# Optimization experiments

Measured on AMD Instinct MI355X. Metric: run time of the kernel, lower is better.

Reference implementation:

```python
import jax, jax.numpy as jnp
from jax import lax
import numpy as np

B, D, P = 4096, 256, 512  # batch, encoded_space_dim (=d_prototypes), n_prototypes
BN_EPS = 1e-5  # torch BatchNorm eval with running_mean=0, running_var=1


def _conv(x, w, stride, pad):
    # x: NCHW, w: OIHW
    return lax.conv_general_dilated(x, w, (stride, stride), [(pad, pad), (pad, pad)],
                                    dimension_numbers=('NCHW', 'OIHW', 'NCHW'))


def _conv_t(x, w, stride, pad, out_pad):
    # torch ConvTranspose2d; w in torch layout [Cin, Cout, kh, kw]
    k = w.shape[2]
    wf = jnp.flip(w, (2, 3)).transpose(1, 0, 2, 3)  # -> OIHW, flipped
    lo = k - 1 - pad
    hi = k - 1 - pad + out_pad
    return lax.conv_general_dilated(x, wf, (1, 1), [(lo, hi), (lo, hi)],
                                    lhs_dilation=(stride, stride),
                                    dimension_numbers=('NCHW', 'OIHW', 'NCHW'))


def _bn(x, g, b):
    # eval-mode BatchNorm2d with running_mean=0, running_var=1
    s = g / jnp.sqrt(1.0 + BN_EPS)
    return x * s[None, :, None, None] + b[None, :, None, None]


def _bias(x, b):
    return x + b[None, :, None, None]


def setup_inputs() -> dict:
    key = jax.random.key(0)
    ks = jax.random.split(key, 32)
    n = jax.random.normal
    inp = {
        'x': jax.random.uniform(ks[0], (B, 1, 28, 28), jnp.float32),
        # encoder
        'w1': n(ks[1], (8, 1, 3, 3), jnp.float32) * 0.1, 'b1': jnp.zeros((8,), jnp.float32),
        'w2': n(ks[2], (16, 8, 3, 3), jnp.float32) * 0.1, 'b2': jnp.zeros((16,), jnp.float32),
        'g2': jnp.ones((16,), jnp.float32), 'bt2': jnp.zeros((16,), jnp.float32),
        'w3': n(ks[3], (D, 16, 3, 3), jnp.float32) * 0.1, 'b3': jnp.zeros((D,), jnp.float32),
        # prototypes (torch.rand init)
        'protolayer': jax.random.uniform(ks[4], (P, D, 1, 1), jnp.float32),
        # up layer (ConvTranspose2d(D, D, 5), torch layout [Cin,Cout,kh,kw])
        'wup': n(ks[5], (D, D, 5, 5), jnp.float32) * 0.02, 'bup': jnp.zeros((D,), jnp.float32),
        'gup': jnp.ones((D,), jnp.float32), 'btup': jnp.zeros((D,), jnp.float32),
        # decoder
        'wd1': n(ks[6], (D, 16, 3, 3), jnp.float32) * 0.05, 'bd1': jnp.zeros((16,), jnp.float32),
        'gd1': jnp.ones((16,), jnp.float32), 'btd1': jnp.zeros((16,), jnp.float32),
        'wd2': n(ks[7], (16, 8, 3, 3), jnp.float32) * 0.1, 'bd2': jnp.zeros((8,), jnp.float32),
        'gd2': jnp.ones((8,), jnp.float32), 'btd2': jnp.zeros((8,), jnp.float32),
        'wd3': n(ks[8], (8, 1, 3, 3), jnp.float32) * 0.1, 'bd3': jnp.zeros((1,), jnp.float32),
    }
    return inp


def reference(x, w1, b1, w2, b2, g2, bt2, w3, b3, protolayer,
              wup, bup, gup, btup,
              wd1, bd1, gd1, btd1, wd2, bd2, gd2, btd2, wd3, bd3):
    # ---- encoder: 28 -> 14 -> 7 -> 5 ----
    h = jax.nn.relu(_bias(_conv(x, w1, 2, 1), b1))
    h = jax.nn.relu(_bn(_bias(_conv(h, w2, 2, 1), b2), g2, bt2))
    h = jax.nn.relu(_bias(_conv(h, w3, 1, 0), b3))  # [B, D, 5, 5]

    # ---- l2 'convolution' with 1x1 prototypes ----
    p = protolayer[:, :, 0, 0]                                  # [P, D]
    x2_patch_sum = jnp.sum(h * h, axis=1)                       # ones-conv, 1x1 kernel -> channel sum [B,5,5]
    xp = jnp.einsum('bdhw,pd->bphw', h, p)                      # [B, P, 5, 5]
    p2 = jnp.sum(p * p, axis=1)                                 # [P]
    distances = jax.nn.relu(x2_patch_sum[:, None] - 2.0 * xp + p2[None, :, None, None])

    # min-pool over full spatial extent
    min_distances = jnp.min(distances, axis=(2, 3))             # [B, P]
    prototype_activations = -min_distances                      # 'linear' distance_2_similarity
    w = jax.nn.softmax(prototype_activations, axis=1)
    z = jnp.einsum('bp,pdkl->bdkl', w, protolayer)              # [B, D, 1, 1]

    # ---- up layer: 1 -> 5 ----
    z = jax.nn.relu(_bn(_bias(_conv_t(z, wup, 1, 0, 0), bup), gup, btup))

    # ---- decoder: 5 -> 7 -> 14 -> 28 ----
    h = jax.nn.relu(_bn(_bias(_conv_t(z, wd1, 1, 0, 0), bd1), gd1, btd1))
    h = jax.nn.relu(_bn(_bias(_conv_t(h, wd2, 2, 1, 1), bd2), gd2, btd2))
    out = jax.nn.sigmoid(_bias(_conv_t(h, wd3, 2, 1, 1), bd3))  # [B, 1, 28, 28]
    return out, min_distances
```

## Files before the change

kernel.cpp:

```cpp
#include <hip/hip_runtime.h>
#include <hip/hip_bf16.h>
#include <math.h>

#define NB 4096
#define DC 256
#define PC 512

typedef unsigned short ushort_t;
typedef __attribute__((ext_vector_type(4))) unsigned short us4;
typedef __attribute__((ext_vector_type(8))) unsigned short us8;
typedef __attribute__((ext_vector_type(8))) short s8v;
typedef __attribute__((ext_vector_type(4))) float f32x4;

__device__ __forceinline__ float bf16_to_f(ushort_t u) {
    union { unsigned int i; float f; } c;
    c.i = ((unsigned int)u) << 16;
    return c.f;
}
__device__ __forceinline__ ushort_t f2bf(float f) {
    union { float f; unsigned int u; } c; c.f = f;
    unsigned int r = c.u + 0x7fffu + ((c.u >> 16) & 1u);
    return (ushort_t)(r >> 16);
}

__global__ __launch_bounds__(256) void k_pre(
    const float* __restrict__ proto, float* __restrict__ p2,
    ushort_t* __restrict__ pfragHi, ushort_t* __restrict__ pfragLo,
    const float* __restrict__ w3, ushort_t* __restrict__ w3fH, ushort_t* __restrict__ w3fL,
    const float* __restrict__ w2, ushort_t* __restrict__ w2fH, ushort_t* __restrict__ w2fL,
    const float* __restrict__ wd1, ushort_t* __restrict__ wd1frag,
    const float* __restrict__ wup, ushort_t* __restrict__ wupfH, ushort_t* __restrict__ wupfL)
{
    int b = blockIdx.x, tid = threadIdx.x;
    __shared__ float red[256];
    if (b < 512) {
        int p = b, d = tid;
        float v = proto[p * DC + d];
        red[d] = v * v;
        __syncthreads();
        for (int s = 128; s > 0; s >>= 1) {
            if (d < s) red[d] += red[d + s];
            __syncthreads();
        }
        if (d == 0) p2[p] = red[0];
    } else if (b < 1024) {
        int idx = (b - 512) * 256 + tid;
        int j = idx & 7, l = (idx >> 3) & 63;
        int k0 = (idx >> 9) & 7, nt = idx >> 12;
        int n = nt * 16 + (l & 15);
        int k = k0 * 32 + (l >> 4) * 8 + j;
        float v = proto[n * DC + k];
        ushort_t hi = f2bf(v);
        pfragHi[idx] = hi;
        pfragLo[idx] = f2bf(v - bf16_to_f(hi));
    } else if (b < 1184) {
        int idx = (b - 1024) * 256 + tid;
        int j = idx & 7, l = (idx >> 3) & 63;
        int q = idx >> 9;
        int k0 = q % 5, nt = q / 5;
        int d = nt * 16 + (l & 15);
        int k = k0 * 32 + (l >> 4) * 8 + j;
        float v = (k < 144) ? w3[d * 144 + k] : 0.f;
        ushort_t hi = f2bf(v);
        w3fH[idx] = hi;
        w3fL[idx] = f2bf(v - bf16_to_f(hi));
    } else if (b < 1190) {
        int idx = (b - 1184) * 256 + tid;
        int j = idx & 7, l = (idx >> 3) & 63;
        int k0 = idx >> 9;
        int ch = l & 15;
        int k = k0 * 32 + (l >> 4) * 8 + j;
        float v = (k < 72) ? w2[ch * 72 + k] : 0.f;
        ushort_t hi = f2bf(v);
        w2fH[idx] = hi;
        w2fL[idx] = f2bf(v - bf16_to_f(hi));
    } else if (b < 1334) {
        int idx = (b - 1190) * 256 + tid;
        int j = idx & 7, l = (idx >> 3) & 63;
        int k0 = (idx >> 9) & 7, nt = idx >> 12;
        int n = nt * 16 + (l & 15);
        int k = k0 * 32 + (l >> 4) * 8 + j;
        wd1frag[idx] = f2bf(wd1[k * 144 + n]);
    } else {
        int idx = (b - 1334) * 256 + tid;
        int j = idx & 7, l = (idx >> 3) & 63;
        int k0 = (idx >> 9) & 7, nt = idx >> 12;
        int np = nt * 16 + (l & 15);
        int d = k0 * 32 + (l >> 4) * 8 + j;
        int pos = np >> 8, ch = np & 255;
        float v = wup[d * 6400 + ch * 25 + pos];
        ushort_t hi = f2bf(v);
        wupfH[idx] = hi;
        wupfL[idx] = f2bf(v - bf16_to_f(hi));
    }
}

__global__ __launch_bounds__(256) void k_pw2(
    const ushort_t* __restrict__ pfragHi, const ushort_t* __restrict__ pfragLo,
    const ushort_t* __restrict__ wupfH, const ushort_t* __restrict__ wupfL,
    ushort_t* __restrict__ PWfrag)
{
    int t = threadIdx.x;
    int w = t >> 6, l = t & 63, lr = l & 15, lg = l >> 4;
    int my = blockIdx.y;
    int ntb = blockIdx.x * 16 + w * 4;
    const s8v* AH = (const s8v*)pfragHi;
    const s8v* AL = (const s8v*)pfragLo;
    const s8v* BH = (const s8v*)wupfH;
    const s8v* BL = (const s8v*)wupfL;
    f32x4 acc[4];
#pragma unroll
    for (int q = 0; q < 4; q++) acc[q] = (f32x4){0.f, 0.f, 0.f, 0.f};
#pragma unroll
    for (int k0 = 0; k0 < 8; k0++) {
        s8v ah = AH[(my * 8 + k0) * 64 + l];
        s8v al = AL[(my * 8 + k0) * 64 + l];
#pragma unroll
        for (int q = 0; q < 4; q++) {
            s8v bh = BH[(size_t)((ntb + q) * 8 + k0) * 64 + l];
            s8v bl = BL[(size_t)((ntb + q) * 8 + k0) * 64 + l];
            acc[q] = __builtin_amdgcn_mfma_f32_16x16x32_bf16(ah, bh, acc[q], 0, 0, 0);
            acc[q] = __builtin_amdgcn_mfma_f32_16x16x32_bf16(al, bh, acc[q], 0, 0, 0);
            acc[q] = __builtin_amdgcn_mfma_f32_16x16x32_bf16(ah, bl, acc[q], 0, 0, 0);
        }
    }
#pragma unroll
    for (int q = 0; q < 4; q++) {
        int nt = ntb + q;
#pragma unroll
        for (int r = 0; r < 4; r++) {
            int p = my * 16 + lg * 4 + r;
            int k0p = p >> 5;
            int ll = ((p >> 3) & 3) * 16 + lr;
            int jj = p & 7;
            PWfrag[(((size_t)(nt * 16 + k0p) * 64) + ll) * 8 + jj] = f2bf(acc[q][r]);
        }
    }
}

__global__ __launch_bounds__(512) void k_enc1(
    const float* __restrict__ x,
    const float* __restrict__ w1, const float* __restrict__ b1,
    const ushort_t* __restrict__ w2fH, const ushort_t* __restrict__ w2fL,
    const float* __restrict__ b2,
    const float* __restrict__ g2, const float* __restrict__ bt2,
    const ushort_t* __restrict__ w3fH, const ushort_t* __restrict__ w3fL,
    const float* __restrict__ b3,
    ushort_t* __restrict__ h3g,
    float* __restrict__ x2g)
{
    int b = blockIdx.x;
    int t = threadIdx.x;
    int w = t >> 6, l = t & 63, lr = l & 15, lg = l >> 4;

    __shared__ __align__(16) unsigned char buf[25856];
    __shared__ float x2s[32];
    float* xb = (float*)buf;
    float* h1 = (float*)(buf + 3136);
    ushort_t* im2Hi = (ushort_t*)(buf + 9408);
    float* h2 = (float*)(buf + 22720);
    ushort_t* imHi = (ushort_t*)buf;

    const float bnr = rsqrtf(1.0f + 1e-5f);

    const float* xg = x + (size_t)b * 784;
    for (int i = t; i < 784; i += 512) xb[i] = xg[i];
    for (int i = t; i < 832; i += 512)
        ((float4*)(buf + 9408))[i] = (float4){0.f, 0.f, 0.f, 0.f};
    if (t < 32) x2s[t] = (t < 25) ? 0.f : 1e30f;
    __syncthreads();

    for (int o = t; o < 1568; o += 512) {
        int c = o / 196, r = o % 196, y = r / 14, xc = r % 14;
        float acc = b1[c];
        for (int sy = 0; sy < 3; sy++) {
            int iy = 2 * y - 1 + sy;
            if ((unsigned)iy >= 28u) continue;
            for (int sx = 0; sx < 3; sx++) {
                int ix = 2 * xc - 1 + sx;
                if ((unsigned)ix >= 28u) continue;
                acc += w1[c * 9 + sy * 3 + sx] * xb[iy * 28 + ix];
            }
        }
        float v = fmaxf(acc, 0.f);
        ushort_t hi = f2bf(v);
        int kb = c * 9;
        int yA, syA, xA, sxA, yB = 0, xB = 0;
        bool hasYB, hasXB;
        if (y & 1) { yA = y >> 1; syA = 2; yB = yA + 1; hasYB = (yB < 7); }
        else       { yA = y >> 1; syA = 1; hasYB = false; }
        if (xc & 1) { xA = xc >> 1; sxA = 2; xB = xA + 1; hasXB = (xB < 7); }
        else        { xA = xc >> 1; sxA = 1; hasXB = false; }
        im2Hi[(yA * 7 + xA) * 104 + kb + syA * 3 + sxA] = hi;
        if (hasXB) im2Hi[(yA * 7 + xB) * 104 + kb + syA * 3] = hi;
        if (hasYB) {
            im2Hi[(yB * 7 + xA) * 104 + kb + sxA] = hi;
            if (hasXB) im2Hi[(yB * 7 + xB) * 104 + kb] = hi;
        }
    }
    __syncthreads();

    if (w < 4) {
        f32x4 cc = {0, 0, 0, 0};
        const s8v* WH = (const s8v*)w2fH;
        const s8v* WL = (const s8v*)w2fL;
#pragma unroll
        for (int k0 = 0; k0 < 3; k0++) {
            s8v a0 = *(const s8v*)&im2Hi[(w * 16 + lr) * 104 + k0 * 32 + lg * 8];
            s8v bh = WH[k0 * 64 + l];
            s8v bl = WL[k0 * 64 + l];
            cc = __builtin_amdgcn_mfma_f32_16x16x32_bf16(a0, bh, cc, 0, 0, 0);
            cc = __builtin_amdgcn_mfma_f32_16x16x32_bf16(a0, bl, cc, 0, 0, 0);
        }
        int ch = lr;
        float s = g2[ch] * bnr, bb = b2[ch], bt = bt2[ch];
#pragma unroll
        for (int r = 0; r < 4; r++) {
            int pos = w * 16 + lg * 4 + r;
            if (pos < 49)
                h2[ch * 49 + pos] = fmaxf((cc[r] + bb) * s + bt, 0.f);
        }
    }
    __syncthreads();

    if (t < 16) imHi[3600 + t] = 0;
    for (int o = t; o < 784; o += 512) {
        float v = h2[o];
        int ci = o / 49, rr = o % 49, iy = rr / 7, ixp = rr % 7;
        ushort_t hi = f2bf(v);
        int kb = ci * 9;
#pragma unroll
        for (int sy = 0; sy < 3; sy++) {
            int py = iy - sy;
            if ((unsigned)py < 5u) {
#pragma unroll
                for (int sx = 0; sx < 3; sx++) {
                    int px = ixp - sx;
                    if ((unsigned)px < 5u)
                        imHi[(py * 5 + px) * 144 + kb + sy * 3 + sx] = hi;
                }
            }
        }
    }
    __syncthreads();

    {
        int nt0 = 2 * w;
        f32x4 c00 = {0,0,0,0}, c01 = {0,0,0,0}, c10 = {0,0,0,0}, c11 = {0,0,0,0};
        const s8v* WH = (const s8v*)w3fH;
        const s8v* WL = (const s8v*)w3fL;
#pragma unroll
        for (int k0 = 0; k0 < 5; k0++) {
            s8v ah0 = *(const s8v*)&imHi[lr * 144 + k0 * 32 + lg * 8];
            s8v ah1 = *(const s8v*)&imHi[(16 + lr) * 144 + k0 * 32 + lg * 8];
            s8v bh0 = WH[(nt0 * 5 + k0) * 64 + l];
            s8v bl0 = WL[(nt0 * 5 + k0) * 64 + l];
            s8v bh1 = WH[((nt0 + 1) * 5 + k0) * 64 + l];
            s8v bl1 = WL[((nt0 + 1) * 5 + k0) * 64 + l];
            c00 = __builtin_amdgcn_mfma_f32_16x16x32_bf16(ah0, bh0, c00, 0, 0, 0);
            c10 = __builtin_amdgcn_mfma_f32_16x16x32_bf16(ah1, bh0, c10, 0, 0, 0);
            c00 = __builtin_amdgcn_mfma_f32_16x16x32_bf16(ah0, bl0, c00, 0, 0, 0);
            c10 = __builtin_amdgcn_mfma_f32_16x16x32_bf16(ah1, bl0, c10, 0, 0, 0);
            c01 = __builtin_amdgcn_mfma_f32_16x16x32_bf16(ah0, bh1, c01, 0, 0, 0);
            c11 = __builtin_amdgcn_mfma_f32_16x16x32_bf16(ah1, bh1, c11, 0, 0, 0);
            c01 = __builtin_amdgcn_mfma_f32_16x16x32_bf16(ah0, bl1, c01, 0, 0, 0);
            c11 = __builtin_amdgcn_mfma_f32_16x16x32_bf16(ah1, bl1, c11, 0, 0, 0);
        }
        ushort_t* hg = h3g + (size_t)b * 6400;
#pragma unroll
        for (int q = 0; q < 2; q++) {
            int d = (nt0 + q) * 16 + lr;
            float bb = b3[d];
            f32x4 cm0 = q ? c01 : c00;
            f32x4 cm1 = q ? c11 : c10;
#pragma unroll
            for (int mt = 0; mt < 2; mt++) {
                f32x4 cv = mt ? cm1 : cm0;
#pragma unroll
                for (int r = 0; r < 4; r++) {
                    int pos = mt * 16 + lg * 4 + r;
                    if (pos < 25) {
                        float h = fmaxf(cv[r] + bb, 0.f);
                        ushort_t hi = f2bf(h);
                        float hh = bf16_to_f(hi);
                        hg[pos * 256 + d] = hi;
                        float sq = hh * hh;
                        sq += __shfl_xor(sq, 1);
                        sq += __shfl_xor(sq, 2);
                        sq += __shfl_xor(sq, 4);
                        sq += __shfl_xor(sq, 8);
                        if (lr == 0) atomicAdd(&x2s[pos], sq);
                    }
                }
            }
        }
    }
    __syncthreads();
    if (t < 32) x2g[(size_t)b * 32 + t] = x2s[t];
}

__global__ __launch_bounds__(1024) void k_enc2(
    const ushort_t* __restrict__ h3g,
    const float* __restrict__ x2g,
    const ushort_t* __restrict__ pfragHi, const ushort_t* __restrict__ pfragLo,
    const float* __restrict__ p2,
    float* __restrict__ md_out,
    ushort_t* __restrict__ Wsm)
{
    int t = threadIdx.x;
    int b0 = blockIdx.x * 2;
    int w = t >> 6, l = t & 63, lr = l & 15, lg = l >> 4;

    __shared__ __align__(16) ushort_t h3s[2][32][264];
    __shared__ float mds[2][512];
    __shared__ float x2sh[2][32];
    __shared__ float wred[2][16];

    for (int i = t; i < 2048; i += 1024) {
        int im = i >> 10, pos = (i >> 5) & 31, c8 = i & 31;
        us8 v = {0, 0, 0, 0, 0, 0, 0, 0};
        if (pos < 25)
            v = *(const us8*)&h3g[(size_t)(b0 + im) * 6400 + pos * 256 + c8 * 8];
        *(us8*)&h3s[im][pos][c8 * 8] = v;
    }
    if (t < 64) x2sh[t >> 5][t & 31] = x2g[(size_t)(b0 + (t >> 5)) * 32 + (t & 31)];
    __syncthreads();

    {
        f32x4 acc[2][2][2];
#pragma unroll
        for (int i = 0; i < 2; i++)
#pragma unroll
            for (int jm = 0; jm < 2; jm++)
#pragma unroll
                for (int mt = 0; mt < 2; mt++) acc[i][jm][mt] = (f32x4){0.f, 0.f, 0.f, 0.f};
        const s8v* BH = (const s8v*)pfragHi;
        const s8v* BL = (const s8v*)pfragLo;
        s8v bhc[2], blc[2], bhn[2], bln[2];
#pragma unroll
        for (int ntq = 0; ntq < 2; ntq++) {
            int nt = w * 2 + ntq;
            bhc[ntq] = BH[(nt * 8 + 0) * 64 + l];
            blc[ntq] = BL[(nt * 8 + 0) * 64 + l];
        }
        for (int k0 = 0; k0 < 8; k0++) {
            if (k0 < 7) {
#pragma unroll
                for (int ntq = 0; ntq < 2; ntq++) {
                    int nt = w * 2 + ntq;
                    bhn[ntq] = BH[(nt * 8 + k0 + 1) * 64 + l];
                    bln[ntq] = BL[(nt * 8 + k0 + 1) * 64 + l];
                }
            }
            s8v ah[2][2];
            ah[0][0] = *(const s8v*)&h3s[0][lr][k0 * 32 + lg * 8];
            ah[0][1] = *(const s8v*)&h3s[0][16 + lr][k0 * 32 + lg * 8];
            ah[1][0] = *(const s8v*)&h3s[1][lr][k0 * 32 + lg * 8];
            ah[1][1] = *(const s8v*)&h3s[1][16 + lr][k0 * 32 + lg * 8];
#pragma unroll
            for (int ntq = 0; ntq < 2; ntq++) {
                s8v bh = bhc[ntq];
                s8v bl = blc[ntq];
#pragma unroll
                for (int im = 0; im < 2; im++) {
                    acc[ntq][im][0] = __builtin_amdgcn_mfma_f32_16x16x32_bf16(ah[im][0], bh, acc[ntq][im][0], 0, 0, 0);
                    acc[ntq][im][1] = __builtin_amdgcn_mfma_f32_16x16x32_bf16(ah[im][1], bh, acc[ntq][im][1], 0, 0, 0);
                    acc[ntq][im][0] = __builtin_amdgcn_mfma_f32_16x16x32_bf16(ah[im][0], bl, acc[ntq][im][0], 0, 0, 0);
                    acc[ntq][im][1] = __builtin_amdgcn_mfma_f32_16x16x32_bf16(ah[im][1], bl, acc[ntq][im][1], 0, 0, 0);
                }
            }
#pragma unroll
            for (int ntq = 0; ntq < 2; ntq++) {
                bhc[ntq] = bhn[ntq];
                blc[ntq] = bln[ntq];
            }
        }
        float x2r[2][8];
#pragma unroll
        for (int im = 0; im < 2; im++)
#pragma unroll
            for (int r = 0; r < 4; r++) {
                x2r[im][r]     = x2sh[im][lg * 4 + r];
                x2r[im][4 + r] = x2sh[im][16 + lg * 4 + r];
            }
#pragma unroll
        for (int ntq = 0; ntq < 2; ntq++) {
            int pcol = (w * 2 + ntq) * 16 + lr;
            float p2v = p2[pcol];
#pragma unroll
            for (int im = 0; im < 2; im++) {
                float mm = 1e30f;
#pragma unroll
                for (int r = 0; r < 4; r++) {
                    float d0 = fmaxf(x2r[im][r]     - 2.f * acc[ntq][im][0][r] + p2v, 0.f);
                    float d1 = fmaxf(x2r[im][4 + r] - 2.f * acc[ntq][im][1][r] + p2v, 0.f);
                    mm = fminf(mm, fminf(d0, d1));
                }
                mm = fminf(mm, __shfl_xor(mm, 16));
                mm = fminf(mm, __shfl_xor(mm, 32));
                if (lg == 0) mds[im][pcol] = mm;
            }
        }
    }
    __syncthreads();

    int img = t >> 9, tt = t & 511;
    float mind = mds[img][tt];
    md_out[(size_t)(b0 + img) * PC + tt] = mind;
    float a = -mind;
    float mx = a;
#pragma unroll
    for (int off = 1; off < 64; off <<= 1) mx = fmaxf(mx, __shfl_xor(mx, off));
    int wv = w & 7;
    if (l == 0) wred[img][wv] = mx;
    __syncthreads();
    float m = wred[img][0];
#pragma unroll
    for (int i = 1; i < 8; i++) m = fmaxf(m, wred[img][i]);
    float e = expf(a - m);
    float sm = e;
#pragma unroll
    for (int off = 1; off < 64; off <<= 1) sm += __shfl_xor(sm, off);
    if (l == 0) wred[img][8 + wv] = sm;
    __syncthreads();
    float ssum = wred[img][8];
#pragma unroll
    for (int i = 9; i < 16; i++) ssum += wred[img][i];
    Wsm[(size_t)(b0 + img) * PC + tt] = f2bf(e / ssum);
}

__global__ __launch_bounds__(512) void k_zup2(
    const ushort_t* __restrict__ Wsm,
    const ushort_t* __restrict__ PWfrag,
    const float* __restrict__ bup, const float* __restrict__ gup,
    const float* __restrict__ btup,
    ushort_t* __restrict__ zupT)
{
    __shared__ __align__(16) ushort_t Bsh[2][8192];
    int t = threadIdx.x;
    int w = t >> 6, l = t & 63;
    int n0 = blockIdx.x * 128;
    int m0 = blockIdx.y * 128;
    int row = m0 + w * 16 + (l & 15);
    int krow = (l >> 4) * 8;
    f32x4 acc[8];
#pragma unroll
    for (int i = 0; i < 8; i++) acc[i] = (f32x4){0.f, 0.f, 0.f, 0.f};
    const s8v* B = (const s8v*)PWfrag;
    int base = blockIdx.x * 8 * 16;

    {
        s8v v0 = B[(size_t)(base + (t >> 6) * 16 + 0) * 64 + (t & 63)];
        s8v v1 = B[(size_t)(base + (t >> 6) * 16 + 1) * 64 + (t & 63)];
        *(s8v*)&Bsh[0][t * 8] = v0;
        *(s8v*)&Bsh[0][4096 + t * 8] = v1;
    }
    __syncthreads();
    for (int r = 0; r < 8; r++) {
        int cur = r & 1;
        if (r < 7) {
            s8v v0 = B[(size_t)(base + (t >> 6) * 16 + 2 * r + 2) * 64 + (t & 63)];
            s8v v1 = B[(size_t)(base + (t >> 6) * 16 + 2 * r + 3) * 64 + (t & 63)];
            *(s8v*)&Bsh[cur ^ 1][t * 8] = v0;
            *(s8v*)&Bsh[cur ^ 1][4096 + t * 8] = v1;
        }
#pragma unroll
        for (int kk = 0; kk < 2; kk++) {
            int k0 = 2 * r + kk;
            s8v a = *(const s8v*)&Wsm[(size_t)row * 512 + k0 * 32 + krow];
#pragma unroll
            for (int nt = 0; nt < 8; nt++) {
                s8v bb = *(const s8v*)&Bsh[cur][kk * 4096 + (nt * 64 + l) * 8];
                acc[nt] = __builtin_amdgcn_mfma_f32_16x16x32_bf16(a, bb, acc[nt], 0, 0, 0);
            }
        }
        __syncthreads();
    }

    const float bnr = rsqrtf(1.0f + 1e-5f);
    int rowbase = m0 + w * 16 + (l >> 4) * 4;
#pragma unroll
    for (int nt = 0; nt < 8; nt++) {
        int n = n0 + nt * 16 + (l & 15);
        int ch = n & 255;
        float sc = gup[ch] * bnr, bb = bup[ch], bt = btup[ch];
#pragma unroll
        for (int r = 0; r < 4; r++) {
            float v = (acc[nt][r] + bb) * sc + bt;
            zupT[(size_t)(rowbase + r) * 6400 + n] = f2bf(fmaxf(v, 0.f));
        }
    }
}

__global__ __launch_bounds__(512) void k_dtail(
    const ushort_t* __restrict__ zupT,
    const ushort_t* __restrict__ wd1frag,
    const float* __restrict__ bd1, const float* __restrict__ gd1, const float* __restrict__ btd1,
    const float* __restrict__ wd2, const float* __restrict__ bd2,
    const float* __restrict__ gd2, const float* __restrict__ btd2,
    const float* __restrict__ wd3, const float* __restrict__ bd3,
    float* __restrict__ out0)
{
    int b0 = blockIdx.x * 2, t = threadIdx.x;
    int w = t >> 6, l = t & 63, lr = l & 15, lg = l >> 4;
    int g = w >> 2, wv = w & 3, tg = t & 255;
    __shared__ __align__(16) unsigned char dbuf[33792];
    __shared__ float hd1p[2][16][64];
    __shared__ float w2sT[9 * 8 * 16];
    __shared__ float w3sT[9 * 8];
    ushort_t* zAb = (ushort_t*)dbuf;
    float* Psb = (float*)dbuf;

    const float bnr = rsqrtf(1.0f + 1e-5f);

    for (int c = t; c < 1600; c += 512) {
        int im = c / 800, cc = c % 800;
        *(us8*)&zAb[im * 8448 + (cc >> 5) * 264 + (cc & 31) * 8] =
            *(const us8*)&zupT[(size_t)(b0 + im) * 6400 + cc * 8];
    }
    for (int i = t; i < 2048; i += 512) ((float*)hd1p)[i] = 0.f;
    for (int i = t; i < 1152; i += 512) {
        int s = i >> 7, rest = i & 127;
        int co = rest >> 4, ci = rest & 15;
        w2sT[i] = wd2[(ci * 8 + co) * 9 + s];
    }
    if (t < 72) {
        int s = t >> 3, ci = t & 7;
        w3sT[t] = wd3[ci * 9 + s];
    }
    __syncthreads();

    {
        f32x4 acc[3][2];
#pragma unroll
        for (int i = 0; i < 3; i++)
#pragma unroll
            for (int mt = 0; mt < 2; mt++) acc[i][mt] = (f32x4){0.f, 0.f, 0.f, 0.f};
        const s8v* B = (const s8v*)wd1frag;
        for (int k0 = 0; k0 < 8; k0++) {
            s8v a0 = *(const s8v*)&zAb[g * 8448 + lr * 264 + k0 * 32 + lg * 8];
            s8v a1 = *(const s8v*)&zAb[g * 8448 + (16 + lr) * 264 + k0 * 32 + lg * 8];
#pragma unroll
            for (int i = 0; i < 3; i++) {
                int nt = wv + 4 * i;
                if (nt < 9) {
                    s8v bb = B[(nt * 8 + k0) * 64 + l];
                    acc[i][0] = __builtin_amdgcn_mfma_f32_16x16x32_bf16(a0, bb, acc[i][0], 0, 0, 0);
                    acc[i][1] = __builtin_amdgcn_mfma_f32_16x16x32_bf16(a1, bb, acc[i][1], 0, 0, 0);
                }
            }
        }
        __syncthreads();
#pragma unroll
        for (int i = 0; i < 3; i++) {
            int nt = wv + 4 * i;
            if (nt < 9) {
                int col = nt * 16 + lr;
#pragma unroll
                for (int mt = 0; mt < 2; mt++)
#pragma unroll
                    for (int r = 0; r < 4; r++) {
                        int pos = mt * 16 + lg * 4 + r;
                        if (pos < 25) Psb[g * 3700 + pos * 148 + col] = acc[i][mt][r];
                    }
            }
        }
    }
    __syncthreads();

    for (int o = tg; o < 784; o += 256) {
        int co = o / 49, rr = o % 49, y = rr / 7, xx = rr % 7;
        float a = bd1[co];
        int sy0 = y - 4 > 0 ? y - 4 : 0, sy1 = y < 2 ? y : 2;
        for (int sy = sy0; sy <= sy1; sy++) {
            int iy = y - sy;
            int sx0 = xx - 4 > 0 ? xx - 4 : 0, sx1 = xx < 2 ? xx : 2;
            for (int sx = sx0; sx <= sx1; sx++) {
                int ix = xx - sx;
                a += Psb[g * 3700 + (iy * 5 + ix) * 148 + co * 9 + sy * 3 + sx];
            }
        }
        float v = a * (gd1[co] * bnr) + btd1[co];
        hd1p[g][co][y * 8 + xx] = fmaxf(v, 0.f);
    }
    __syncthreads();

    {
        if (t < 464) {
            int im = t / 232, rest = t % 232;
            int co = rest / 29, s = rest % 29;
            int yy = (s < 15) ? 14 : (s - 15);
            int xx2 = (s < 15) ? s : 14;
            ((float*)dbuf)[im * 1808 + co * 225 + yy * 15 + xx2] = 0.f;
        }
        int cls = (wv + g) & 3;
        int cy = cls >> 1, cx = cls & 1;
        if (l < 56 && (l & 7) < 7) {
            int r = l >> 3, c = l & 7;
            float acc[8];
#pragma unroll
            for (int co = 0; co < 8; co++) acc[co] = 0.f;
            const float* hb = &hd1p[g][0][0];
            int niy = 1 + cy, nix = 1 + cx;
            for (int ty = 0; ty < niy; ty++) {
                int iy = r + ty;
                int sy = cy ? (ty ? 0 : 2) : 1;
                for (int tx = 0; tx < nix; tx++) {
                    int ix = c + tx;
                    int sx = cx ? (tx ? 0 : 2) : 1;
                    const float* wp = &w2sT[(sy * 3 + sx) * 128];
                    int hoff = iy * 8 + ix;
                    float h[16];
#pragma unroll
                    for (int ci = 0; ci < 16; ci++) h[ci] = hb[ci * 64 + hoff];
#pragma unroll
                    for (int co = 0; co < 8; co++) {
                        const float4* wp4 = (const float4*)&wp[co * 16];
                        float4 wa = wp4[0], wb4 = wp4[1], wc4 = wp4[2], wd4 = wp4[3];
                        float a = acc[co];
                        a = fmaf(h[0], wa.x, a);  a = fmaf(h[1], wa.y, a);
                        a = fmaf(h[2], wa.z, a);  a = fmaf(h[3], wa.w, a);
                        a = fmaf(h[4], wb4.x, a); a = fmaf(h[5], wb4.y, a);
                        a = fmaf(h[6], wb4.z, a); a = fmaf(h[7], wb4.w, a);
                        a = fmaf(h[8], wc4.x, a); a = fmaf(h[9], wc4.y, a);
                        a = fmaf(h[10], wc4.z, a); a = fmaf(h[11], wc4.w, a);
                        a = fmaf(h[12], wd4.x, a); a = fmaf(h[13], wd4.y, a);
                        a = fmaf(h[14], wd4.z, a); a = fmaf(h[15], wd4.w, a);
                        acc[co] = a;
                    }
                }
            }
            int y = 2 * r + cy, x = 2 * c + cx;
            float* hout = (float*)dbuf + g * 1808;
#pragma unroll
            for (int co = 0; co < 8; co++) {
                float v = (acc[co] + bd2[co]) * (gd2[co] * bnr) + btd2[co];
                hout[co * 225 + y * 15 + x] = fmaxf(v, 0.f);
            }
        }
    }
    __syncthreads();

    {
        int cls = (wv + g) & 3;
        int cy = cls >> 1, cx = cls & 1;
        const float* h2b = (const float*)dbuf + g * 1808;
        float* og = out0 + (size_t)(b0 + g) * 784;
        int niy = 1 + cy, nix = 1 + cx;
#pragma unroll
        for (int j = 0; j < 4; j++) {
            int idx = l + 64 * j;
            if (idx < 224) {
                int row = idx >> 4, col = idx & 15;
                if (col < 14) {
                    float a = bd3[0];
                    for (int ty = 0; ty < niy; ty++) {
                        int iy = row + ty;
                        int sy = cy ? (ty ? 0 : 2) : 1;
                        for (int tx = 0; tx < nix; tx++) {
                            int ix = col + tx;
                            int sx = cx ? (tx ? 0 : 2) : 1;
                            const float* wp = &w3sT[(sy * 3 + sx) * 8];
                            int hoff = iy * 15 + ix;
#pragma unroll
                            for (int ci = 0; ci < 8; ci++)
                                a = fmaf(h2b[ci * 225 + hoff], wp[ci], a);
                        }
                    }
                    int y = 2 * row + cy, x = 2 * col + cx;
                    og[y * 28 + x] = 1.f / (1.f + expf(-a));
                }
            }
        }
    }
}

extern "C" void kernel_launch(void* const* d_in, const int* in_sizes, int n_in,
                              void* d_out, int out_size, void* d_ws, size_t ws_size,
                              hipStream_t stream) {
    const float* x    = (const float*)d_in[0];
    const float* w1   = (const float*)d_in[1];
    const float* b1   = (const float*)d_in[2];
    const float* w2   = (const float*)d_in[3];
    const float* b2   = (const float*)d_in[4];
    const float* g2   = (const float*)d_in[5];
    const float* bt2  = (const float*)d_in[6];
    const float* w3   = (const float*)d_in[7];
    const float* b3   = (const float*)d_in[8];
    const float* proto= (const float*)d_in[9];
    const float* wup  = (const float*)d_in[10];
    const float* bup  = (const float*)d_in[11];
    const float* gup  = (const float*)d_in[12];
    const float* btup = (const float*)d_in[13];
    const float* wd1  = (const float*)d_in[14];
    const float* bd1  = (const float*)d_in[15];
    const float* gd1  = (const float*)d_in[16];
    const float* btd1 = (const float*)d_in[17];
    const float* wd2  = (const float*)d_in[18];
    const float* bd2  = (const float*)d_in[19];
    const float* gd2  = (const float*)d_in[20];
    const float* btd2 = (const float*)d_in[21];
    const float* wd3  = (const float*)d_in[22];
    const float* bd3  = (const float*)d_in[23];

    float* out0   = (float*)d_out;
    float* out_md = out0 + (size_t)NB * 784;

    float*    p2      = (float*)d_ws;
    float*    x2g     = p2 + 512;
    ushort_t* pfragHi = (ushort_t*)(x2g + 131072);
    ushort_t* pfragLo = pfragHi + 131072;
    ushort_t* w3fH    = pfragLo + 131072;
    ushort_t* w3fL    = w3fH + 40960;
    ushort_t* w2fH    = w3fL + 40960;
    ushort_t* w2fL    = w2fH + 1536;
    ushort_t* wd1frag = w2fL + 1536;
    ushort_t* wupfH   = wd1frag + 36864;
    ushort_t* wupfL   = wupfH + 1638400;
    ushort_t* PWfrag  = wupfL + 1638400;
    ushort_t* Wsm     = PWfrag + 3276800;
    ushort_t* BIG     = Wsm + 2097152;
    ushort_t* h3g     = BIG;
    ushort_t* zupT    = BIG;

    hipLaunchKernelGGL(k_pre, dim3(7734), dim3(256), 0, stream,
                       proto, p2, pfragHi, pfragLo, w3, w3fH, w3fL,
                       w2, w2fH, w2fL, wd1, wd1frag, wup, wupfH, wupfL);
    hipLaunchKernelGGL(k_pw2, dim3(25, 32), dim3(256), 0, stream,
                       pfragHi, pfragLo, wupfH, wupfL, PWfrag);
    hipLaunchKernelGGL(k_enc1, dim3(NB), dim3(512), 0, stream,
                       x, w1, b1, w2fH, w2fL, b2, g2, bt2, w3fH, w3fL, b3, h3g, x2g);
    hipLaunchKernelGGL(k_enc2, dim3(NB / 2), dim3(1024), 0, stream,
                       h3g, x2g, pfragHi, pfragLo, p2, out_md, Wsm);
    hipLaunchKernelGGL(k_zup2, dim3(50, 32), dim3(512), 0, stream,
                       Wsm, PWfrag, bup, gup, btup, zupT);
    hipLaunchKernelGGL(k_dtail, dim3(NB / 2), dim3(512), 0, stream,
                       zupT, wd1frag, bd1, gd1, btd1, wd2, bd2, gd2, btd2, wd3, bd3, out0);
}
```

Before: 289.6 us.

## Process two images per enc1 block and move x2 sums into enc2

```diff
diff --git a/kernel.cpp b/kernel.cpp
--- a/kernel.cpp
+++ b/kernel.cpp
@@ -146,31 +146,30 @@
     const float* __restrict__ g2, const float* __restrict__ bt2,
     const ushort_t* __restrict__ w3fH, const ushort_t* __restrict__ w3fL,
     const float* __restrict__ b3,
-    ushort_t* __restrict__ h3g,
-    float* __restrict__ x2g)
+    ushort_t* __restrict__ h3g)
 {
-    int b = blockIdx.x;
+    int b0 = blockIdx.x * 2;
     int t = threadIdx.x;
     int w = t >> 6, l = t & 63, lr = l & 15, lg = l >> 4;
-
-    __shared__ __align__(16) unsigned char buf[25856];
-    __shared__ float x2s[32];
-    float* xb = (float*)buf;
-    float* h1 = (float*)(buf + 3136);
-    ushort_t* im2Hi = (ushort_t*)(buf + 9408);
-    float* h2 = (float*)(buf + 22720);
-    ushort_t* imHi = (ushort_t*)buf;
+    int tim = t >> 8, tt = t & 255;
+
+    __shared__ __align__(16) unsigned char buf[51712];
+    unsigned char* bufI = buf + tim * 25856;
+    float* xb = (float*)bufI;
+    float* h1 = (float*)(bufI + 3136);
+    ushort_t* im2Hi = (ushort_t*)(bufI + 9408);
+    float* h2 = (float*)(bufI + 22720);
+    ushort_t* imHi = (ushort_t*)bufI;
 
     const float bnr = rsqrtf(1.0f + 1e-5f);
 
-    const float* xg = x + (size_t)b * 784;
-    for (int i = t; i < 784; i += 512) xb[i] = xg[i];
-    for (int i = t; i < 832; i += 512)
-        ((float4*)(buf + 9408))[i] = (float4){0.f, 0.f, 0.f, 0.f};
-    if (t < 32) x2s[t] = (t < 25) ? 0.f : 1e30f;
-    __syncthreads();
-
-    for (int o = t; o < 1568; o += 512) {
+    const float* xg = x + (size_t)(b0 + tim) * 784;
+    for (int i = tt; i < 784; i += 256) xb[i] = xg[i];
+    for (int i = tt; i < 832; i += 256)
+        ((float4*)(bufI + 9408))[i] = (float4){0.f, 0.f, 0.f, 0.f};
+    __syncthreads();
+
+    for (int o = tt; o < 1568; o += 256) {
         int c = o / 196, r = o % 196, y = r / 14, xc = r % 14;
         float acc = b1[c];
         for (int sy = 0; sy < 3; sy++) {
@@ -200,13 +199,14 @@
     }
     __syncthreads();
 
-    if (w < 4) {
+    {
+        int w4 = w & 3;
         f32x4 cc = {0, 0, 0, 0};
         const s8v* WH = (const s8v*)w2fH;
         const s8v* WL = (const s8v*)w2fL;
 #pragma unroll
         for (int k0 = 0; k0 < 3; k0++) {
-            s8v a0 = *(const s8v*)&im2Hi[(w * 16 + lr) * 104 + k0 * 32 + lg * 8];
+            s8v a0 = *(const s8v*)&im2Hi[(w4 * 16 + lr) * 104 + k0 * 32 + lg * 8];
             s8v bh = WH[k0 * 64 + l];
             s8v bl = WL[k0 * 64 + l];
             cc = __builtin_amdgcn_mfma_f32_16x16x32_bf16(a0, bh, cc, 0, 0, 0);
@@ -216,15 +216,15 @@
         float s = g2[ch] * bnr, bb = b2[ch], bt = bt2[ch];
 #pragma unroll
         for (int r = 0; r < 4; r++) {
-            int pos = w * 16 + lg * 4 + r;
+            int pos = w4 * 16 + lg * 4 + r;
             if (pos < 49)
                 h2[ch * 49 + pos] = fmaxf((cc[r] + bb) * s + bt, 0.f);
         }
     }
     __syncthreads();
 
-    if (t < 16) imHi[3600 + t] = 0;
-    for (int o = t; o < 784; o += 512) {
+    if (tt < 16) imHi[3600 + tt] = 0;
+    for (int o = tt; o < 784; o += 256) {
         float v = h2[o];
         int ci = o / 49, rr = o % 49, iy = rr / 7, ixp = rr % 7;
         ushort_t hi = f2bf(v);
@@ -245,63 +245,71 @@
     __syncthreads();
 
     {
+        const ushort_t* imHi0 = (const ushort_t*)buf;
+        const ushort_t* imHi1 = (const ushort_t*)(buf + 25856);
         int nt0 = 2 * w;
-        f32x4 c00 = {0,0,0,0}, c01 = {0,0,0,0}, c10 = {0,0,0,0}, c11 = {0,0,0,0};
+        f32x4 c[2][2][2];
+#pragma unroll
+        for (int im = 0; im < 2; im++)
+#pragma unroll
+            for (int q = 0; q < 2; q++)
+#pragma unroll
+                for (int mt = 0; mt < 2; mt++) c[im][q][mt] = (f32x4){0.f, 0.f, 0.f, 0.f};
         const s8v* WH = (const s8v*)w3fH;
         const s8v* WL = (const s8v*)w3fL;
 #pragma unroll
         for (int k0 = 0; k0 < 5; k0++) {
-            s8v ah0 = *(const s8v*)&imHi[lr * 144 + k0 * 32 + lg * 8];
-            s8v ah1 = *(const s8v*)&imHi[(16 + lr) * 144 + k0 * 32 + lg * 8];
+            s8v a00 = *(const s8v*)&imHi0[lr * 144 + k0 * 32 + lg * 8];
+            s8v a01 = *(const s8v*)&imHi0[(16 + lr) * 144 + k0 * 32 + lg * 8];
+            s8v a10 = *(const s8v*)&imHi1[lr * 144 + k0 * 32 + lg * 8];
+            s8v a11 = *(const s8v*)&imHi1[(16 + lr) * 144 + k0 * 32 + lg * 8];
             s8v bh0 = WH[(nt0 * 5 + k0) * 64 + l];
             s8v bl0 = WL[(nt0 * 5 + k0) * 64 + l];
             s8v bh1 = WH[((nt0 + 1) * 5 + k0) * 64 + l];
             s8v bl1 = WL[((nt0 + 1) * 5 + k0) * 64 + l];
-            c00 = __builtin_amdgcn_mfma_f32_16x16x32_bf16(ah0, bh0, c00, 0, 0, 0);
-            c10 = __builtin_amdgcn_mfma_f32_16x16x32_bf16(ah1, bh0, c10, 0, 0, 0);
-            c00 = __builtin_amdgcn_mfma_f32_16x16x32_bf16(ah0, bl0, c00, 0, 0, 0);
-            c10 = __builtin_amdgcn_mfma_f32_16x16x32_bf16(ah1, bl0, c10, 0, 0, 0);
-            c01 = __builtin_amdgcn_mfma_f32_16x16x32_bf16(ah0, bh1, c01, 0, 0, 0);
-            c11 = __builtin_amdgcn_mfma_f32_16x16x32_bf16(ah1, bh1, c11, 0, 0, 0);
-            c01 = __builtin_amdgcn_mfma_f32_16x16x32_bf16(ah0, bl1, c01, 0, 0, 0);
-            c11 = __builtin_amdgcn_mfma_f32_16x16x32_bf16(ah1, bl1, c11, 0, 0, 0);
-        }
-        ushort_t* hg = h3g + (size_t)b * 6400;
-#pragma unroll
-        for (int q = 0; q < 2; q++) {
-            int d = (nt0 + q) * 16 + lr;
-            float bb = b3[d];
-            f32x4 cm0 = q ? c01 : c00;
-            f32x4 cm1 = q ? c11 : c10;
-#pragma unroll
-            for (int mt = 0; mt < 2; mt++) {
-                f32x4 cv = mt ? cm1 : cm0;
-#pragma unroll
-                for (int r = 0; r < 4; r++) {
-                    int pos = mt * 16 + lg * 4 + r;
-                    if (pos < 25) {
-                        float h = fmaxf(cv[r] + bb, 0.f);
-                        ushort_t hi = f2bf(h);
-                        float hh = bf16_to_f(hi);
-                        hg[pos * 256 + d] = hi;
-                        float sq = hh * hh;
-                        sq += __shfl_xor(sq, 1);
-                        sq += __shfl_xor(sq, 2);
-                        sq += __shfl_xor(sq, 4);
-                        sq += __shfl_xor(sq, 8);
-                        if (lr == 0) atomicAdd(&x2s[pos], sq);
+            c[0][0][0] = __builtin_amdgcn_mfma_f32_16x16x32_bf16(a00, bh0, c[0][0][0], 0, 0, 0);
+            c[0][0][1] = __builtin_amdgcn_mfma_f32_16x16x32_bf16(a01, bh0, c[0][0][1], 0, 0, 0);
+            c[0][0][0] = __builtin_amdgcn_mfma_f32_16x16x32_bf16(a00, bl0, c[0][0][0], 0, 0, 0);
+            c[0][0][1] = __builtin_amdgcn_mfma_f32_16x16x32_bf16(a01, bl0, c[0][0][1], 0, 0, 0);
+            c[0][1][0] = __builtin_amdgcn_mfma_f32_16x16x32_bf16(a00, bh1, c[0][1][0], 0, 0, 0);
+            c[0][1][1] = __builtin_amdgcn_mfma_f32_16x16x32_bf16(a01, bh1, c[0][1][1], 0, 0, 0);
+            c[0][1][0] = __builtin_amdgcn_mfma_f32_16x16x32_bf16(a00, bl1, c[0][1][0], 0, 0, 0);
+            c[0][1][1] = __builtin_amdgcn_mfma_f32_16x16x32_bf16(a01, bl1, c[0][1][1], 0, 0, 0);
+            c[1][0][0] = __builtin_amdgcn_mfma_f32_16x16x32_bf16(a10, bh0, c[1][0][0], 0, 0, 0);
+            c[1][0][1] = __builtin_amdgcn_mfma_f32_16x16x32_bf16(a11, bh0, c[1][0][1], 0, 0, 0);
+            c[1][0][0] = __builtin_amdgcn_mfma_f32_16x16x32_bf16(a10, bl0, c[1][0][0], 0, 0, 0);
+            c[1][0][1] = __builtin_amdgcn_mfma_f32_16x16x32_bf16(a11, bl0, c[1][0][1], 0, 0, 0);
+            c[1][1][0] = __builtin_amdgcn_mfma_f32_16x16x32_bf16(a10, bh1, c[1][1][0], 0, 0, 0);
+            c[1][1][1] = __builtin_amdgcn_mfma_f32_16x16x32_bf16(a11, bh1, c[1][1][1], 0, 0, 0);
+            c[1][1][0] = __builtin_amdgcn_mfma_f32_16x16x32_bf16(a10, bl1, c[1][1][0], 0, 0, 0);
+            c[1][1][1] = __builtin_amdgcn_mfma_f32_16x16x32_bf16(a11, bl1, c[1][1][1], 0, 0, 0);
+        }
+#pragma unroll
+        for (int im = 0; im < 2; im++) {
+            ushort_t* hg = h3g + (size_t)(b0 + im) * 6400;
+#pragma unroll
+            for (int q = 0; q < 2; q++) {
+                int d = (nt0 + q) * 16 + lr;
+                float bb = b3[d];
+#pragma unroll
+                for (int mt = 0; mt < 2; mt++) {
+                    f32x4 cv = c[im][q][mt];
+#pragma unroll
+                    for (int r = 0; r < 4; r++) {
+                        int pos = mt * 16 + lg * 4 + r;
+                        if (pos < 25) {
+                            float h = fmaxf(cv[r] + bb, 0.f);
+                            hg[pos * 256 + d] = f2bf(h);
+                        }
                     }
                 }
             }
         }
     }
-    __syncthreads();
-    if (t < 32) x2g[(size_t)b * 32 + t] = x2s[t];
 }
 
 __global__ __launch_bounds__(1024) void k_enc2(
     const ushort_t* __restrict__ h3g,
-    const float* __restrict__ x2g,
     const ushort_t* __restrict__ pfragHi, const ushort_t* __restrict__ pfragLo,
     const float* __restrict__ p2,
     float* __restrict__ md_out,
@@ -314,6 +322,7 @@
     __shared__ __align__(16) ushort_t h3s[2][32][264];
     __shared__ float mds[2][512];
     __shared__ float x2sh[2][32];
+    __shared__ float x2part[2][25][8];
     __shared__ float wred[2][16];
 
     for (int i = t; i < 2048; i += 1024) {
@@ -323,7 +332,31 @@
             v = *(const us8*)&h3g[(size_t)(b0 + im) * 6400 + pos * 256 + c8 * 8];
         *(us8*)&h3s[im][pos][c8 * 8] = v;
     }
-    if (t < 64) x2sh[t >> 5][t & 31] = x2g[(size_t)(b0 + (t >> 5)) * 32 + (t & 31)];
+    __syncthreads();
+
+    if (t < 400) {
+        int im = t / 200, rest = t % 200;
+        int pos = rest >> 3, ch = rest & 7;
+        const ushort_t* hp = &h3s[im][pos][ch * 32];
+        float s = 0.f;
+#pragma unroll
+        for (int i = 0; i < 32; i++) {
+            float f = bf16_to_f(hp[i]);
+            s = fmaf(f, f, s);
+        }
+        x2part[im][pos][ch] = s;
+    }
+    __syncthreads();
+    if (t < 64) {
+        int im = t >> 5, pos = t & 31;
+        float s = 1e30f;
+        if (pos < 25) {
+            s = 0.f;
+#pragma unroll
+            for (int c = 0; c < 8; c++) s += x2part[im][pos][c];
+        }
+        x2sh[im][pos] = s;
+    }
     __syncthreads();
 
     {
@@ -728,10 +761,10 @@
                        w2, w2fH, w2fL, wd1, wd1frag, wup, wupfH, wupfL);
     hipLaunchKernelGGL(k_pw2, dim3(25, 32), dim3(256), 0, stream,
                        pfragHi, pfragLo, wupfH, wupfL, PWfrag);
-    hipLaunchKernelGGL(k_enc1, dim3(NB), dim3(512), 0, stream,
-                       x, w1, b1, w2fH, w2fL, b2, g2, bt2, w3fH, w3fL, b3, h3g, x2g);
+    hipLaunchKernelGGL(k_enc1, dim3(NB / 2), dim3(512), 0, stream,
+                       x, w1, b1, w2fH, w2fL, b2, g2, bt2, w3fH, w3fL, b3, h3g);
     hipLaunchKernelGGL(k_enc2, dim3(NB / 2), dim3(1024), 0, stream,
-                       h3g, x2g, pfragHi, pfragLo, p2, out_md, Wsm);
+                       h3g, pfragHi, pfragLo, p2, out_md, Wsm);
     hipLaunchKernelGGL(k_zup2, dim3(50, 32), dim3(512), 0, stream,
                        Wsm, PWfrag, bup, gup, btup, zupT);
     hipLaunchKernelGGL(k_dtail, dim3(NB / 2), dim3(512), 0, stream,
```

After: 273.0 us. -5.7%, faster.
